# Performance work log

Hardware: AMD Instinct MI355X
Metric: run time of the kernel (lower is better)

The kernel has to match this reference:

```python
import jax, jax.numpy as jnp
import numpy as np

NUM_BLOCKS = 100  # original samples at most 100 blocks; ids are in [0, NUM_BLOCKS)
EPS = 1e-8       # F.cosine_similarity default eps (clamps norms from below)


def setup_inputs() -> dict:
    key = jax.random.key(0)
    k1, k2 = jax.random.split(key)
    N, D = 1000000, 128
    z = jax.random.normal(k1, (N, D), dtype=jnp.float32)
    poi_to_road_block = jax.random.randint(k2, (N,), 0, NUM_BLOCKS, dtype=jnp.int32)
    return {"z": z, "poi_to_road_block": poi_to_road_block}


def reference(z, poi_to_road_block):
    N, D = z.shape
    ids = poi_to_road_block
    # per-block counts and sums -> block centers (mean embedding per road block)
    counts = jax.ops.segment_sum(jnp.ones((N,), z.dtype), ids, num_segments=NUM_BLOCKS)  # [B]
    sums = jax.ops.segment_sum(z, ids, num_segments=NUM_BLOCKS)                          # [B, D]
    centers = sums / jnp.maximum(counts, 1.0)[:, None]                                   # [B, D]
    # cosine similarity between each point and its block center
    c = centers[ids]                                                                     # [N, D] gather
    dot = jnp.sum(z * c, axis=-1)                                                        # [N]
    z_norm = jnp.maximum(jnp.sqrt(jnp.sum(z * z, axis=-1)), EPS)
    c_norm = jnp.maximum(jnp.sqrt(jnp.sum(c * c, axis=-1)), EPS)
    cos = dot / (z_norm * c_norm)                                                        # [N]
    # per-block mean cosine, then average (1 - mean_cos) over blocks with >1 member
    cos_sum = jax.ops.segment_sum(cos, ids, num_segments=NUM_BLOCKS)                     # [B]
    mean_cos = cos_sum / jnp.maximum(counts, 1.0)
    valid = counts > 1.0
    total = jnp.sum(jnp.where(valid, 1.0 - mean_cos, 0.0))
    count = jnp.maximum(jnp.sum(valid.astype(z.dtype)), 1.0)
    return total / count
```

## Files before the change

### kernel.cpp

```cpp
#include <hip/hip_runtime.h>
#include <hip/hip_bf16.h>

#define NBLK 100
#define DIM 128
#define EVEC (NBLK * DIM)
#define SLICE (2 * EVEC + NBLK)
#define EPSV 1e-8f
#define SSCALE 4194304.0f
#define NSCALE 16777216.0f
#define INV_SSCALE (1.0f / SSCALE)
#define INV_NSCALE (1.0f / NSCALE)
#define PPART 8

__global__ __launch_bounds__(1024) void rbc_accum(
    const float4* __restrict__ z4, const int* __restrict__ ids,
    float* __restrict__ ws, int N, int nwaves) {
  __shared__ int lsum[EVEC];
  __shared__ int lnsum[EVEC];
  __shared__ int lcnt[NBLK];
  const int tid = threadIdx.x;
  for (int e = tid; e < EVEC; e += 1024) { lsum[e] = 0; lnsum[e] = 0; }
  if (tid < NBLK) lcnt[tid] = 0;
  __syncthreads();

  const int lane = tid & 63;
  const int q  = lane >> 4;
  const int r  = lane & 15;
  const int qp = q & 1;
  const int w = blockIdx.x * (blockDim.x >> 6) + (tid >> 6);
  const int ngroups = N >> 2;

#define RBC_POINT_BODY(A0, A1, BB)                                           \
  {                                                                          \
    float sq = A0.x * A0.x + A0.y * A0.y + A0.z * A0.z + A0.w * A0.w +       \
               A1.x * A1.x + A1.y * A1.y + A1.z * A1.z + A1.w * A1.w;        \
    _Pragma("unroll")                                                        \
    for (int m = 1; m < 16; m <<= 1) sq += __shfl_xor(sq, m);                \
    const float rn = 1.0f / fmaxf(sqrtf(sq), EPSV);                          \
    const float v0[4] = {A0.x, A0.y, A0.z, A0.w};                            \
    const float v1[4] = {A1.x, A1.y, A1.z, A1.w};                            \
    const int base = BB * DIM;                                               \
    _Pragma("unroll")                                                        \
    for (int s = 0; s < 4; ++s) {                                            \
      const float x0 = qp ? v0[s ^ 1] : v0[s];                               \
      const float x1 = qp ? v1[s ^ 1] : v1[s];                               \
      const int p0 = base + r + ((((s & 1) ^ qp)) << 4) + ((s >> 1) << 5);   \
      atomicAdd(&lsum[p0], __float2int_rn(x0 * SSCALE));                     \
      atomicAdd(&lnsum[p0], __float2int_rn(x0 * rn * NSCALE));               \
      atomicAdd(&lsum[p0 + 64], __float2int_rn(x1 * SSCALE));                \
      atomicAdd(&lnsum[p0 + 64], __float2int_rn(x1 * rn * NSCALE));          \
    }                                                                        \
    if (r == 0) atomicAdd(&lcnt[BB], 1);                                     \
  }

  int j = w;
  for (; j + nwaves < ngroups; j += (nwaves << 1)) {
    const int jB = j + nwaves;
    const int iA = (j << 2) + q;
    const int iB = (jB << 2) + q;
    const float4* zpA = z4 + ((size_t)iA << 5);
    const float4* zpB = z4 + ((size_t)iB << 5);
    const float4 a0 = zpA[r];
    const float4 a1 = zpA[r + 16];
    const float4 b0 = zpB[r];
    const float4 b1 = zpB[r + 16];
    const int bA = ids[iA];
    const int bB = ids[iB];
    RBC_POINT_BODY(a0, a1, bA);
    RBC_POINT_BODY(b0, b1, bB);
  }
  if (j < ngroups) {
    const int iA = (j << 2) + q;
    const float4* zpA = z4 + ((size_t)iA << 5);
    const float4 a0 = zpA[r];
    const float4 a1 = zpA[r + 16];
    const int bA = ids[iA];
    RBC_POINT_BODY(a0, a1, bA);
  }
  if (blockIdx.x == 0 && (tid >> 6) == 0 && (N & 3)) {
    const int i = (ngroups << 2) + q;
    if (q < (N & 3)) {
      const float4* zp = z4 + ((size_t)i << 5);
      const float4 a0 = zp[r];
      const float4 a1 = zp[r + 16];
      const int b = ids[i];
      RBC_POINT_BODY(a0, a1, b);
    }
  }
#undef RBC_POINT_BODY
  __syncthreads();

  float* slice = ws + (size_t)blockIdx.x * SLICE;
  for (int e = tid; e < EVEC; e += 1024) {
    slice[e] = (float)lsum[e] * INV_SSCALE;
    slice[EVEC + e] = (float)lnsum[e] * INV_NSCALE;
  }
  if (tid < NBLK) slice[2 * EVEC + tid] = (float)lcnt[tid];
}

__global__ void rbc_reduce1(const float* __restrict__ ws,
                            float* __restrict__ part, int G, int GP) {
  const int e = blockIdx.x * 256 + threadIdx.x;
  if (e >= SLICE) return;
  const int p = blockIdx.y;
  float s = 0.f;
  const int g0 = p * GP;
  const int g1 = (g0 + GP < G) ? (g0 + GP) : G;
  for (int g = g0; g < g1; ++g) s += ws[(size_t)g * SLICE + e];
  part[(size_t)p * SLICE + e] = s;
}

__global__ __launch_bounds__(1024) void rbc_final(const float* __restrict__ part,
                                                  float* __restrict__ out) {
  __shared__ float mres[NBLK];
  __shared__ float vld[NBLK];
  const int tid = threadIdx.x;
  const int wave = tid >> 6, lane = tid & 63;
  for (int b = wave; b < NBLK; b += 16) {
    float s0 = 0.f, s1 = 0.f, n0 = 0.f, n1 = 0.f, cnt = 0.f;
#pragma unroll
    for (int p = 0; p < PPART; ++p) {
      const float* f = part + (size_t)p * SLICE;
      s0 += f[b * DIM + lane];
      s1 += f[b * DIM + 64 + lane];
      n0 += f[EVEC + b * DIM + lane];
      n1 += f[EVEC + b * DIM + 64 + lane];
      cnt += f[2 * EVEC + b];
    }
    float S2 = s0 * s0 + s1 * s1;
    float ND = n0 * s0 + n1 * s1;
#pragma unroll
    for (int m = 1; m < 64; m <<= 1) {
      S2 += __shfl_xor(S2, m);
      ND += __shfl_xor(ND, m);
    }
    if (lane == 0) {
      const float cnt1 = fmaxf(cnt, 1.0f);
      const float cn = fmaxf(sqrtf(S2) / cnt1, EPSV);
      const float mean_cos = ND / (cnt1 * cnt1 * cn);
      const bool valid = cnt > 1.0f;
      mres[b] = valid ? (1.0f - mean_cos) : 0.f;
      vld[b] = valid ? 1.0f : 0.f;
    }
  }
  __syncthreads();
  if (tid < 64) {
    float t = (tid < NBLK ? mres[tid] : 0.f) +
              (tid + 64 < NBLK ? mres[tid + 64] : 0.f);
    float c = (tid < NBLK ? vld[tid] : 0.f) +
              (tid + 64 < NBLK ? vld[tid + 64] : 0.f);
#pragma unroll
    for (int m = 1; m < 64; m <<= 1) {
      t += __shfl_xor(t, m);
      c += __shfl_xor(c, m);
    }
    if (tid == 0) out[0] = t / fmaxf(c, 1.0f);
  }
}

extern "C" void kernel_launch(void* const* d_in, const int* in_sizes, int n_in,
                              void* d_out, int out_size, void* d_ws, size_t ws_size,
                              hipStream_t stream) {
  const float* z = (const float*)d_in[0];
  const int* ids = (const int*)d_in[1];
  const int N = in_sizes[1];
  float* out = (float*)d_out;
  float* ws = (float*)d_ws;

  size_t cap = ws_size / (sizeof(float) * (size_t)SLICE);
  int G = 256;
  if (cap < (size_t)(G + PPART)) {
    G = (int)cap - PPART;
    if (G < 1) G = 1;
  }
  const int nwaves = G * (1024 / 64);
  const int GP = (G + PPART - 1) / PPART;

  rbc_accum<<<G, 1024, 0, stream>>>((const float4*)z, ids, ws, N, nwaves);

  float* part = ws + (size_t)G * SLICE;
  dim3 rgrid((SLICE + 255) / 256, PPART);
  rbc_reduce1<<<rgrid, 256, 0, stream>>>(ws, part, G, GP);
  rbc_final<<<1, 1024, 0, stream>>>(part, out);
}
```

Baseline: 123.6 us.

## Replace two-stage partial reduction with per-block stat kernel

Removes the old two-stage tail, where a generic column-sum kernel over G slices was followed by a single-block finalize that summed partials. One workgroup per road block now sums that block's 128-dim sum and normalized-sum vectors plus its count over all G slices. It reduces them to the dot-product and squared-norm scalars in shared memory, and a tiny 128-thread kernel combines the 100 block stats. This spreads the post-accumulation reduction across 100 workgroups and shrinks the final kernel, at the cost of strided reads across slices within each workgroup.

New measurement: 125.0 us. About the same (+1.1%).

```diff
diff --git a/kernel.cpp b/kernel.cpp
--- a/kernel.cpp
+++ b/kernel.cpp
@@ -10,7 +10,6 @@
 #define NSCALE 16777216.0f
 #define INV_SSCALE (1.0f / SSCALE)
 #define INV_NSCALE (1.0f / NSCALE)
-#define PPART 8
 
 __global__ __launch_bounds__(1024) void rbc_accum(
     const float4* __restrict__ z4, const int* __restrict__ ids,
@@ -98,64 +97,82 @@
   if (tid < NBLK) slice[2 * EVEC + tid] = (float)lcnt[tid];
 }
 
-__global__ void rbc_reduce1(const float* __restrict__ ws,
-                            float* __restrict__ part, int G, int GP) {
-  const int e = blockIdx.x * 256 + threadIdx.x;
-  if (e >= SLICE) return;
-  const int p = blockIdx.y;
-  float s = 0.f;
-  const int g0 = p * GP;
-  const int g1 = (g0 + GP < G) ? (g0 + GP) : G;
-  for (int g = g0; g < g1; ++g) s += ws[(size_t)g * SLICE + e];
-  part[(size_t)p * SLICE + e] = s;
-}
+__global__ __launch_bounds__(512) void rbc_blockstat(
+    const float* __restrict__ ws, float* __restrict__ stat, int G) {
+  __shared__ float sp[512];
+  __shared__ float np_[512];
+  const int b = blockIdx.x;
+  const int t = threadIdx.x;
+  const int d = t & 127;
+  const int qq = t >> 7;
+  const int gpq = (G + 3) >> 2;
+  const int g0 = qq * gpq;
+  const int g1 = (g0 + gpq < G) ? (g0 + gpq) : G;
+  float s = 0.f, n = 0.f;
+  for (int g = g0; g < g1; ++g) {
+    const float* f = ws + (size_t)g * SLICE + (size_t)b * DIM;
+    s += f[d];
+    n += f[EVEC + d];
+  }
+  sp[t] = s;
+  np_[t] = n;
 
-__global__ __launch_bounds__(1024) void rbc_final(const float* __restrict__ part,
-                                                  float* __restrict__ out) {
-  __shared__ float mres[NBLK];
-  __shared__ float vld[NBLK];
-  const int tid = threadIdx.x;
-  const int wave = tid >> 6, lane = tid & 63;
-  for (int b = wave; b < NBLK; b += 16) {
-    float s0 = 0.f, s1 = 0.f, n0 = 0.f, n1 = 0.f, cnt = 0.f;
+  if (t >= 256 && t < 320) {
+    const int l = t - 256;
+    float c = 0.f;
+    for (int g = l; g < G; g += 64) c += ws[(size_t)g * SLICE + 2 * EVEC + b];
 #pragma unroll
-    for (int p = 0; p < PPART; ++p) {
-      const float* f = part + (size_t)p * SLICE;
-      s0 += f[b * DIM + lane];
-      s1 += f[b * DIM + 64 + lane];
-      n0 += f[EVEC + b * DIM + lane];
-      n1 += f[EVEC + b * DIM + 64 + lane];
-      cnt += f[2 * EVEC + b];
-    }
-    float S2 = s0 * s0 + s1 * s1;
-    float ND = n0 * s0 + n1 * s1;
+    for (int m = 1; m < 64; m <<= 1) c += __shfl_xor(c, m);
+    if (l == 0) stat[b * 4 + 2] = c;
+  }
+  __syncthreads();
+
+  if (t < 128) {
+    const float ss = sp[t] + sp[t + 128] + sp[t + 256] + sp[t + 384];
+    const float nn = np_[t] + np_[t + 128] + np_[t + 256] + np_[t + 384];
+    sp[t] = ss * ss;
+    np_[t] = nn * ss;
+  }
+  __syncthreads();
+
+  if (t < 64) {
+    float S2 = sp[t] + sp[t + 64];
+    float ND = np_[t] + np_[t + 64];
 #pragma unroll
     for (int m = 1; m < 64; m <<= 1) {
       S2 += __shfl_xor(S2, m);
       ND += __shfl_xor(ND, m);
     }
-    if (lane == 0) {
-      const float cnt1 = fmaxf(cnt, 1.0f);
-      const float cn = fmaxf(sqrtf(S2) / cnt1, EPSV);
-      const float mean_cos = ND / (cnt1 * cnt1 * cn);
-      const bool valid = cnt > 1.0f;
-      mres[b] = valid ? (1.0f - mean_cos) : 0.f;
-      vld[b] = valid ? 1.0f : 0.f;
+    if (t == 0) {
+      stat[b * 4 + 0] = ND;
+      stat[b * 4 + 1] = S2;
     }
   }
+}
+
+__global__ __launch_bounds__(128) void rbc_final(const float* __restrict__ stat,
+                                                 float* __restrict__ out) {
+  __shared__ float lv[2];
+  __shared__ float lc[2];
+  const int t = threadIdx.x;
+  float val = 0.f, vc = 0.f;
+  if (t < NBLK) {
+    const float ND = stat[t * 4 + 0];
+    const float S2 = stat[t * 4 + 1];
+    const float cnt = stat[t * 4 + 2];
+    const float cnt1 = fmaxf(cnt, 1.0f);
+    const float cn = fmaxf(sqrtf(S2) / cnt1, EPSV);
+    const float mean_cos = ND / (cnt1 * cnt1 * cn);
+    if (cnt > 1.0f) { val = 1.0f - mean_cos; vc = 1.0f; }
+  }
+#pragma unroll
+  for (int m = 1; m < 64; m <<= 1) {
+    val += __shfl_xor(val, m);
+    vc += __shfl_xor(vc, m);
+  }
+  if ((t & 63) == 0) { lv[t >> 6] = val; lc[t >> 6] = vc; }
   __syncthreads();
-  if (tid < 64) {
-    float t = (tid < NBLK ? mres[tid] : 0.f) +
-              (tid + 64 < NBLK ? mres[tid + 64] : 0.f);
-    float c = (tid < NBLK ? vld[tid] : 0.f) +
-              (tid + 64 < NBLK ? vld[tid + 64] : 0.f);
-#pragma unroll
-    for (int m = 1; m < 64; m <<= 1) {
-      t += __shfl_xor(t, m);
-      c += __shfl_xor(c, m);
-    }
-    if (tid == 0) out[0] = t / fmaxf(c, 1.0f);
-  }
+  if (t == 0) out[0] = (lv[0] + lv[1]) / fmaxf(lc[0] + lc[1], 1.0f);
 }
 
 extern "C" void kernel_launch(void* const* d_in, const int* in_sizes, int n_in,
@@ -167,19 +184,14 @@
   float* out = (float*)d_out;
   float* ws = (float*)d_ws;
 
-  size_t cap = ws_size / (sizeof(float) * (size_t)SLICE);
+  size_t cap = (ws_size - 400 * sizeof(float)) / (sizeof(float) * (size_t)SLICE);
   int G = 256;
-  if (cap < (size_t)(G + PPART)) {
-    G = (int)cap - PPART;
-    if (G < 1) G = 1;
-  }
+  if (cap < (size_t)G) G = (int)(cap > 1 ? cap : 1);
   const int nwaves = G * (1024 / 64);
-  const int GP = (G + PPART - 1) / PPART;
 
   rbc_accum<<<G, 1024, 0, stream>>>((const float4*)z, ids, ws, N, nwaves);
 
-  float* part = ws + (size_t)G * SLICE;
-  dim3 rgrid((SLICE + 255) / 256, PPART);
-  rbc_reduce1<<<rgrid, 256, 0, stream>>>(ws, part, G, GP);
-  rbc_final<<<1, 1024, 0, stream>>>(part, out);
+  float* stat = ws + (size_t)G * SLICE;
+  rbc_blockstat<<<NBLK, 512, 0, stream>>>(ws, stat, G);
+  rbc_final<<<1, 128, 0, stream>>>(stat, out);
 }
```
